# Performance work log

Hardware: AMD Instinct MI355X
Metric: run time of the kernel (lower is better)

## Reference

```python
import jax, jax.numpy as jnp
import numpy as np


def setup_inputs() -> dict:
    key = jax.random.key(0)
    k1, k2, k3 = jax.random.split(key, 3)
    B, H, W, D, K = 16, 32, 32, 128, 32
    x = jax.random.normal(k1, (B, H, W, D), dtype=jnp.float32)
    std = 1.0 / (K * D) ** 0.5
    codewords = jax.random.uniform(k2, (K, D), minval=-std, maxval=std, dtype=jnp.float32)
    scale = jax.random.uniform(k3, (K,), minval=-1.0, maxval=0.0, dtype=jnp.float32)
    return {"x": x, "codewords": codewords, "scale": scale}


def reference(x, codewords, scale):
    B, H, W, D = x.shape
    K = codewords.shape[0]
    X = x.reshape(B, H * W, D)                      # [B, N, D]
    # scaled squared distances: s_k * ||x_n - c_k||^2 via expansion (no BNKD tensor)
    x2 = jnp.sum(X * X, axis=-1, keepdims=True)     # [B, N, 1]
    c2 = jnp.sum(codewords * codewords, axis=-1)    # [K]
    xc = jnp.einsum('bnd,kd->bnk', X, codewords)    # [B, N, K]
    SL = scale[None, None, :] * (x2 - 2.0 * xc + c2[None, None, :])
    A = jax.nn.softmax(SL, axis=2)                  # assignment weights [B, N, K]
    # E_bk = sum_n A_bnk * (x_bn - c_k)
    E = jnp.einsum('bnk,bnd->bkd', A, X) - jnp.sum(A, axis=1)[:, :, None] * codewords[None]
    return E
```

## Files before the change

### kernel.cpp

```cpp
#include <hip/hip_runtime.h>


constexpr int NPB = 32;
constexpr int XS  = 132;

__global__ __launch_bounds__(256)
void enc_partial(const float* __restrict__ x, const float* __restrict__ cw,
                 const float* __restrict__ scale, float* __restrict__ ws)
{
    __shared__ float x_s[NPB * XS];
    __shared__ float A_s[NPB * 32];
    __shared__ float x2_s[NPB];
    __shared__ float asum_s[4 * 32];

    const int tid = threadIdx.x;
    const int b   = blockIdx.x >> 5;
    const int s   = blockIdx.x & 31;

    const float4* xg4 = (const float4*)(x + (size_t)(b * 1024 + s * NPB) * 128);
#pragma unroll
    for (int i = 0; i < 4; ++i) {
        int f = tid + 256 * i;
        float4 v = xg4[f];
        *(float4*)&x_s[(f >> 5) * XS + (f & 31) * 4] = v;
    }

    const int lane = tid & 63;
    const int k    = lane & 31;
    const int h    = lane >> 5;
    const int w    = tid >> 6;

    float4 cf[16];
    const float4* cw4 = (const float4*)(cw + k * 128 + h * 64);
    float c2a = 0.f, c2b = 0.f;
#pragma unroll
    for (int i = 0; i < 16; i += 2) {
        float4 c0 = cw4[i], c1 = cw4[i + 1];
        cf[i] = c0; cf[i + 1] = c1;
        c2a += c0.x * c0.x + c0.y * c0.y + c0.z * c0.z + c0.w * c0.w;
        c2b += c1.x * c1.x + c1.y * c1.y + c1.z * c1.z + c1.w * c1.w;
    }
    float c2 = c2a + c2b;
    c2 += __shfl_xor(c2, 32);
    const float sck = scale[k];

    __syncthreads();

    {
        int p = tid >> 3, q = tid & 7;
        float ss = 0.f;
#pragma unroll
        for (int i = 0; i < 4; ++i) {
            float4 v = *(const float4*)&x_s[p * XS + q * 16 + 4 * i];
            ss += v.x * v.x + v.y * v.y + v.z * v.z + v.w * v.w;
        }
        ss += __shfl_xor(ss, 1);
        ss += __shfl_xor(ss, 2);
        ss += __shfl_xor(ss, 4);
        if (q == 0) x2_s[p] = ss;
    }
    __syncthreads();

    float a_part = 0.f;
#pragma unroll
    for (int p = 0; p < 8; ++p) {
        const int n = (w << 3) + p;
        const float4* xr = (const float4*)&x_s[n * XS + h * 64];
        float xc0 = 0.f, xc1 = 0.f, xc2 = 0.f, xc3 = 0.f;
#pragma unroll
        for (int i = 0; i < 16; i += 4) {
            float4 v0 = xr[i + 0], v1 = xr[i + 1], v2 = xr[i + 2], v3 = xr[i + 3];
            xc0 += v0.x * cf[i+0].x + v0.y * cf[i+0].y + v0.z * cf[i+0].z + v0.w * cf[i+0].w;
            xc1 += v1.x * cf[i+1].x + v1.y * cf[i+1].y + v1.z * cf[i+1].z + v1.w * cf[i+1].w;
            xc2 += v2.x * cf[i+2].x + v2.y * cf[i+2].y + v2.z * cf[i+2].z + v2.w * cf[i+2].w;
            xc3 += v3.x * cf[i+3].x + v3.y * cf[i+3].y + v3.z * cf[i+3].z + v3.w * cf[i+3].w;
        }
        float xc = (xc0 + xc1) + (xc2 + xc3);
        xc += __shfl_xor(xc, 32);

        float sl = sck * (x2_s[n] - 2.f * xc + c2);
        float m = sl;
#pragma unroll
        for (int msk = 16; msk >= 1; msk >>= 1) m = fmaxf(m, __shfl_xor(m, msk));
        float e = __expf(sl - m);
        float den = e;
#pragma unroll
        for (int msk = 16; msk >= 1; msk >>= 1) den += __shfl_xor(den, msk);
        float a = e / den;
        A_s[n * 32 + k] = a;
        a_part += a;
    }
    if (h == 0) asum_s[w * 32 + k] = a_part;
    __syncthreads();

    {
        const int kg = tid >> 5;
        const int dg = tid & 31;
        float acc[4][4];
#pragma unroll
        for (int i = 0; i < 4; ++i)
#pragma unroll
            for (int j = 0; j < 4; ++j) acc[i][j] = 0.f;

#pragma unroll 8
        for (int n = 0; n < NPB; ++n) {
            float4 a4 = *(const float4*)&A_s[n * 32 + kg * 4];
            float4 x4 = *(const float4*)&x_s[n * XS + dg * 4];
            acc[0][0] += a4.x * x4.x; acc[0][1] += a4.x * x4.y;
            acc[0][2] += a4.x * x4.z; acc[0][3] += a4.x * x4.w;
            acc[1][0] += a4.y * x4.x; acc[1][1] += a4.y * x4.y;
            acc[1][2] += a4.y * x4.z; acc[1][3] += a4.y * x4.w;
            acc[2][0] += a4.z * x4.x; acc[2][1] += a4.z * x4.y;
            acc[2][2] += a4.z * x4.z; acc[2][3] += a4.z * x4.w;
            acc[3][0] += a4.w * x4.x; acc[3][1] += a4.w * x4.y;
            acc[3][2] += a4.w * x4.z; acc[3][3] += a4.w * x4.w;
        }

        float as[4];
#pragma unroll
        for (int i = 0; i < 4; ++i)
            as[i] = asum_s[kg * 4 + i] + asum_s[32 + kg * 4 + i] +
                    asum_s[64 + kg * 4 + i] + asum_s[96 + kg * 4 + i];

        float* wb = ws + (size_t)(b * 32 + s) * 4096;
#pragma unroll
        for (int i = 0; i < 4; ++i) {
            const int kk = kg * 4 + i;
            float4 c4 = *(const float4*)&cw[kk * 128 + dg * 4];
            float4 r;
            r.x = acc[i][0] - as[i] * c4.x;
            r.y = acc[i][1] - as[i] * c4.y;
            r.z = acc[i][2] - as[i] * c4.z;
            r.w = acc[i][3] - as[i] * c4.w;
            *(float4*)&wb[kk * 128 + dg * 4] = r;
        }
    }
}

__global__ __launch_bounds__(256)
void enc_reduce(const float* __restrict__ ws, float* __restrict__ out)
{
    const int gid = blockIdx.x * 256 + threadIdx.x;
    const int b   = gid >> 10;
    const int j4  = gid & 1023;
    const float4* base = (const float4*)ws + (size_t)b * 32768 + j4;
    float4 a0 = {0,0,0,0}, a1 = {0,0,0,0}, a2 = {0,0,0,0}, a3 = {0,0,0,0};
#pragma unroll
    for (int s = 0; s < 32; s += 4) {
        float4 v0 = base[(size_t)(s + 0) * 1024];
        float4 v1 = base[(size_t)(s + 1) * 1024];
        float4 v2 = base[(size_t)(s + 2) * 1024];
        float4 v3 = base[(size_t)(s + 3) * 1024];
        a0.x += v0.x; a0.y += v0.y; a0.z += v0.z; a0.w += v0.w;
        a1.x += v1.x; a1.y += v1.y; a1.z += v1.z; a1.w += v1.w;
        a2.x += v2.x; a2.y += v2.y; a2.z += v2.z; a2.w += v2.w;
        a3.x += v3.x; a3.y += v3.y; a3.z += v3.z; a3.w += v3.w;
    }
    float4 r;
    r.x = (a0.x + a1.x) + (a2.x + a3.x);
    r.y = (a0.y + a1.y) + (a2.y + a3.y);
    r.z = (a0.z + a1.z) + (a2.z + a3.z);
    r.w = (a0.w + a1.w) + (a2.w + a3.w);
    ((float4*)out)[gid] = r;
}

extern "C" void kernel_launch(void* const* d_in, const int* in_sizes, int n_in,
                              void* d_out, int out_size, void* d_ws, size_t ws_size,
                              hipStream_t stream)
{
    const float* x     = (const float*)d_in[0];
    const float* cw    = (const float*)d_in[1];
    const float* scale = (const float*)d_in[2];
    float* out = (float*)d_out;
    float* ws  = (float*)d_ws;

    enc_partial<<<512, 256, 0, stream>>>(x, cw, scale, ws);
    enc_reduce<<<64, 256, 0, stream>>>(ws, out);
}
```

Baseline: 75.94 us.

## Compute distance GEMM with register-tiled shared-memory codewords and split-D partial sums

Codewords are staged in shared memory instead of held per-thread in registers. The x·c product becomes a register-tiled 4x4 outer-product GEMM, with D split across four groups whose partial sums go to shared memory and are reduced afterwards. Softmax runs per point with 8 threads each covering 4 codewords, so fewer shuffles are needed, and the assignment sums are folded into the second GEMM loop. This trades roughly 33KB more shared memory and an extra barrier for fewer registers and better reuse in the first GEMM.

```diff
diff --git a/kernel.cpp b/kernel.cpp
--- a/kernel.cpp
+++ b/kernel.cpp
@@ -1,109 +1,131 @@
 #include <hip/hip_runtime.h>
 
 
-constexpr int NPB = 32;
-constexpr int XS  = 132;
+constexpr int XS = 132;
 
 __global__ __launch_bounds__(256)
 void enc_partial(const float* __restrict__ x, const float* __restrict__ cw,
                  const float* __restrict__ scale, float* __restrict__ ws)
 {
-    __shared__ float x_s[NPB * XS];
-    __shared__ float A_s[NPB * 32];
-    __shared__ float x2_s[NPB];
-    __shared__ float asum_s[4 * 32];
+    __shared__ float x_s[32 * XS];
+    __shared__ float c_s[32 * XS];
+    __shared__ float S_s[4 * 32 * 32];
+    __shared__ float A_s[32 * 32];
+    __shared__ float x2_s[32];
+    __shared__ float c2_s[32];
 
     const int tid = threadIdx.x;
     const int b   = blockIdx.x >> 5;
     const int s   = blockIdx.x & 31;
 
-    const float4* xg4 = (const float4*)(x + (size_t)(b * 1024 + s * NPB) * 128);
+    const float4* xg4 = (const float4*)(x + (size_t)(b * 1024 + s * 32) * 128);
+    const float4* cg4 = (const float4*)cw;
 #pragma unroll
     for (int i = 0; i < 4; ++i) {
         int f = tid + 256 * i;
-        float4 v = xg4[f];
-        *(float4*)&x_s[(f >> 5) * XS + (f & 31) * 4] = v;
+        float4 vx = xg4[f];
+        float4 vc = cg4[f];
+        *(float4*)&x_s[(f >> 5) * XS + (f & 31) * 4] = vx;
+        *(float4*)&c_s[(f >> 5) * XS + (f & 31) * 4] = vc;
     }
-
-    const int lane = tid & 63;
-    const int k    = lane & 31;
-    const int h    = lane >> 5;
-    const int w    = tid >> 6;
-
-    float4 cf[16];
-    const float4* cw4 = (const float4*)(cw + k * 128 + h * 64);
-    float c2a = 0.f, c2b = 0.f;
-#pragma unroll
-    for (int i = 0; i < 16; i += 2) {
-        float4 c0 = cw4[i], c1 = cw4[i + 1];
-        cf[i] = c0; cf[i + 1] = c1;
-        c2a += c0.x * c0.x + c0.y * c0.y + c0.z * c0.z + c0.w * c0.w;
-        c2b += c1.x * c1.x + c1.y * c1.y + c1.z * c1.z + c1.w * c1.w;
-    }
-    float c2 = c2a + c2b;
-    c2 += __shfl_xor(c2, 32);
-    const float sck = scale[k];
-
     __syncthreads();
 
     {
-        int p = tid >> 3, q = tid & 7;
-        float ss = 0.f;
+        const int p = tid >> 3, q = tid & 7;
+        float sx = 0.f, sc = 0.f;
 #pragma unroll
         for (int i = 0; i < 4; ++i) {
             float4 v = *(const float4*)&x_s[p * XS + q * 16 + 4 * i];
-            ss += v.x * v.x + v.y * v.y + v.z * v.z + v.w * v.w;
+            float4 c = *(const float4*)&c_s[p * XS + q * 16 + 4 * i];
+            sx += v.x * v.x + v.y * v.y + v.z * v.z + v.w * v.w;
+            sc += c.x * c.x + c.y * c.y + c.z * c.z + c.w * c.w;
         }
-        ss += __shfl_xor(ss, 1);
-        ss += __shfl_xor(ss, 2);
-        ss += __shfl_xor(ss, 4);
-        if (q == 0) x2_s[p] = ss;
+        sx += __shfl_xor(sx, 1); sc += __shfl_xor(sc, 1);
+        sx += __shfl_xor(sx, 2); sc += __shfl_xor(sc, 2);
+        sx += __shfl_xor(sx, 4); sc += __shfl_xor(sc, 4);
+        if (q == 0) { x2_s[p] = sx; c2_s[p] = sc; }
     }
     __syncthreads();
 
-    float a_part = 0.f;
+    {
+        const int dq = tid >> 6;
+        const int kg = (tid >> 3) & 7;
+        const int ng = tid & 7;
+        float acc[4][4];
 #pragma unroll
-    for (int p = 0; p < 8; ++p) {
-        const int n = (w << 3) + p;
-        const float4* xr = (const float4*)&x_s[n * XS + h * 64];
-        float xc0 = 0.f, xc1 = 0.f, xc2 = 0.f, xc3 = 0.f;
+        for (int r = 0; r < 4; ++r)
 #pragma unroll
-        for (int i = 0; i < 16; i += 4) {
-            float4 v0 = xr[i + 0], v1 = xr[i + 1], v2 = xr[i + 2], v3 = xr[i + 3];
-            xc0 += v0.x * cf[i+0].x + v0.y * cf[i+0].y + v0.z * cf[i+0].z + v0.w * cf[i+0].w;
-            xc1 += v1.x * cf[i+1].x + v1.y * cf[i+1].y + v1.z * cf[i+1].z + v1.w * cf[i+1].w;
-            xc2 += v2.x * cf[i+2].x + v2.y * cf[i+2].y + v2.z * cf[i+2].z + v2.w * cf[i+2].w;
-            xc3 += v3.x * cf[i+3].x + v3.y * cf[i+3].y + v3.z * cf[i+3].z + v3.w * cf[i+3].w;
+            for (int c = 0; c < 4; ++c) acc[r][c] = 0.f;
+
+#pragma unroll
+        for (int i = 0; i < 8; ++i) {
+            const int d4 = dq * 8 + i;
+            float4 xv[4], cv[4];
+#pragma unroll
+            for (int r = 0; r < 4; ++r) {
+                xv[r] = *(const float4*)&x_s[(ng * 4 + r) * XS + d4 * 4];
+                cv[r] = *(const float4*)&c_s[(kg * 4 + r) * XS + d4 * 4];
+            }
+#pragma unroll
+            for (int r = 0; r < 4; ++r)
+#pragma unroll
+                for (int c = 0; c < 4; ++c)
+                    acc[r][c] += xv[r].x * cv[c].x + xv[r].y * cv[c].y +
+                                 xv[r].z * cv[c].z + xv[r].w * cv[c].w;
         }
-        float xc = (xc0 + xc1) + (xc2 + xc3);
-        xc += __shfl_xor(xc, 32);
+#pragma unroll
+        for (int r = 0; r < 4; ++r) {
+            float4 o = {acc[r][0], acc[r][1], acc[r][2], acc[r][3]};
+            *(float4*)&S_s[(dq * 32 + ng * 4 + r) * 32 + kg * 4] = o;
+        }
+    }
+    __syncthreads();
 
-        float sl = sck * (x2_s[n] - 2.f * xc + c2);
-        float m = sl;
+    {
+        const int n = tid >> 3, j = tid & 7;
+        float4 xc = {0.f, 0.f, 0.f, 0.f};
 #pragma unroll
-        for (int msk = 16; msk >= 1; msk >>= 1) m = fmaxf(m, __shfl_xor(m, msk));
-        float e = __expf(sl - m);
-        float den = e;
-#pragma unroll
-        for (int msk = 16; msk >= 1; msk >>= 1) den += __shfl_xor(den, msk);
-        float a = e / den;
-        A_s[n * 32 + k] = a;
-        a_part += a;
+        for (int dq = 0; dq < 4; ++dq) {
+            float4 v = *(const float4*)&S_s[(dq * 32 + n) * 32 + j * 4];
+            xc.x += v.x; xc.y += v.y; xc.z += v.z; xc.w += v.w;
+        }
+        const float4 s4  = ((const float4*)scale)[j];
+        const float4 c24 = *(const float4*)&c2_s[j * 4];
+        const float x2n  = x2_s[n];
+        float4 sl;
+        sl.x = s4.x * (x2n - 2.f * xc.x + c24.x);
+        sl.y = s4.y * (x2n - 2.f * xc.y + c24.y);
+        sl.z = s4.z * (x2n - 2.f * xc.z + c24.z);
+        sl.w = s4.w * (x2n - 2.f * xc.w + c24.w);
+        float m = fmaxf(fmaxf(sl.x, sl.y), fmaxf(sl.z, sl.w));
+        m = fmaxf(m, __shfl_xor(m, 1));
+        m = fmaxf(m, __shfl_xor(m, 2));
+        m = fmaxf(m, __shfl_xor(m, 4));
+        float4 e;
+        e.x = __expf(sl.x - m); e.y = __expf(sl.y - m);
+        e.z = __expf(sl.z - m); e.w = __expf(sl.w - m);
+        float den = (e.x + e.y) + (e.z + e.w);
+        den += __shfl_xor(den, 1);
+        den += __shfl_xor(den, 2);
+        den += __shfl_xor(den, 4);
+        const float rd = 1.f / den;
+        float4 a = {e.x * rd, e.y * rd, e.z * rd, e.w * rd};
+        *(float4*)&A_s[n * 32 + j * 4] = a;
     }
-    if (h == 0) asum_s[w * 32 + k] = a_part;
     __syncthreads();
 
     {
         const int kg = tid >> 5;
         const int dg = tid & 31;
         float acc[4][4];
+        float as[4] = {0.f, 0.f, 0.f, 0.f};
 #pragma unroll
         for (int i = 0; i < 4; ++i)
 #pragma unroll
             for (int j = 0; j < 4; ++j) acc[i][j] = 0.f;
 
 #pragma unroll 8
-        for (int n = 0; n < NPB; ++n) {
+        for (int n = 0; n < 32; ++n) {
             float4 a4 = *(const float4*)&A_s[n * 32 + kg * 4];
             float4 x4 = *(const float4*)&x_s[n * XS + dg * 4];
             acc[0][0] += a4.x * x4.x; acc[0][1] += a4.x * x4.y;
@@ -114,13 +136,8 @@
             acc[2][2] += a4.z * x4.z; acc[2][3] += a4.z * x4.w;
             acc[3][0] += a4.w * x4.x; acc[3][1] += a4.w * x4.y;
             acc[3][2] += a4.w * x4.z; acc[3][3] += a4.w * x4.w;
+            as[0] += a4.x; as[1] += a4.y; as[2] += a4.z; as[3] += a4.w;
         }
-
-        float as[4];
-#pragma unroll
-        for (int i = 0; i < 4; ++i)
-            as[i] = asum_s[kg * 4 + i] + asum_s[32 + kg * 4 + i] +
-                    asum_s[64 + kg * 4 + i] + asum_s[96 + kg * 4 + i];
 
         float* wb = ws + (size_t)(b * 32 + s) * 4096;
 #pragma unroll
```

Measured after the change: 71.87 us. 1.06x faster.

## Compute x·codeword distances with bf16 MFMA instead of scalar FP32 dot products

Applied to the files above, without the earlier changes.

The block converts its x tile and the codewords to bf16 in shared memory and computes the 32x32 x·c product with a single-wave-shaped 32x32x16 bf16 MFMA chain. Each wave then takes four rows of the accumulator for the softmax. The x and codeword squared norms are computed at load time. The per-k assignment sums are now accumulated in the second matmul loop, replacing the separate shared array. This cuts FP32 FMA and register-held codeword work in the first stage, at the cost of bf16 rounding in the distance logits and redundant MFMA work across the four waves.

```diff
diff --git a/kernel.cpp b/kernel.cpp
--- a/kernel.cpp
+++ b/kernel.cpp
@@ -1,126 +1,125 @@
 #include <hip/hip_runtime.h>
 
 
-constexpr int NPB = 32;
+typedef __attribute__((ext_vector_type(8))) short bf16x8;
+typedef __attribute__((ext_vector_type(16))) float f32x16;
+
 constexpr int XS  = 132;
+constexpr int XBS = 136;
+
+__device__ __forceinline__ unsigned short f2bf(float f) {
+    unsigned u = __float_as_uint(f);
+    u += 0x7fffu + ((u >> 16) & 1u);
+    return (unsigned short)(u >> 16);
+}
 
 __global__ __launch_bounds__(256)
 void enc_partial(const float* __restrict__ x, const float* __restrict__ cw,
                  const float* __restrict__ scale, float* __restrict__ ws)
 {
-    __shared__ float x_s[NPB * XS];
-    __shared__ float A_s[NPB * 32];
-    __shared__ float x2_s[NPB];
-    __shared__ float asum_s[4 * 32];
+    __shared__ float          x_s[32 * XS];
+    __shared__ unsigned short xb_s[32 * XBS];
+    __shared__ unsigned short cb_s[32 * XBS];
+    __shared__ float          A_s[32 * 32];
+    __shared__ float          x2_s[32];
+    __shared__ float          c2_s[32];
 
     const int tid = threadIdx.x;
     const int b   = blockIdx.x >> 5;
     const int s   = blockIdx.x & 31;
 
-    const float4* xg4 = (const float4*)(x + (size_t)(b * 1024 + s * NPB) * 128);
+    const float4* xg4 = (const float4*)(x + (size_t)(b * 1024 + s * 32) * 128);
+    const float4* cg4 = (const float4*)cw;
+
 #pragma unroll
     for (int i = 0; i < 4; ++i) {
-        int f = tid + 256 * i;
-        float4 v = xg4[f];
-        *(float4*)&x_s[(f >> 5) * XS + (f & 31) * 4] = v;
-    }
-
-    const int lane = tid & 63;
-    const int k    = lane & 31;
-    const int h    = lane >> 5;
-    const int w    = tid >> 6;
-
-    float4 cf[16];
-    const float4* cw4 = (const float4*)(cw + k * 128 + h * 64);
-    float c2a = 0.f, c2b = 0.f;
+        const int f   = tid + 256 * i;
+        const int row = 8 * i + (tid >> 5);
+        const int col = tid & 31;
+        float4 vx = xg4[f];
+        float4 vc = cg4[f];
+        *(float4*)&x_s[row * XS + col * 4] = vx;
+        short4 hx = { (short)f2bf(vx.x), (short)f2bf(vx.y),
+                      (short)f2bf(vx.z), (short)f2bf(vx.w) };
+        short4 hc = { (short)f2bf(vc.x), (short)f2bf(vc.y),
+                      (short)f2bf(vc.z), (short)f2bf(vc.w) };
+        *(short4*)&xb_s[row * XBS + col * 4] = hx;
+        *(short4*)&cb_s[row * XBS + col * 4] = hc;
+        float sx = vx.x * vx.x + vx.y * vx.y + vx.z * vx.z + vx.w * vx.w;
+        float sc = vc.x * vc.x + vc.y * vc.y + vc.z * vc.z + vc.w * vc.w;
 #pragma unroll
-    for (int i = 0; i < 16; i += 2) {
-        float4 c0 = cw4[i], c1 = cw4[i + 1];
-        cf[i] = c0; cf[i + 1] = c1;
-        c2a += c0.x * c0.x + c0.y * c0.y + c0.z * c0.z + c0.w * c0.w;
-        c2b += c1.x * c1.x + c1.y * c1.y + c1.z * c1.z + c1.w * c1.w;
-    }
-    float c2 = c2a + c2b;
-    c2 += __shfl_xor(c2, 32);
-    const float sck = scale[k];
-
-    __syncthreads();
-
-    {
-        int p = tid >> 3, q = tid & 7;
-        float ss = 0.f;
-#pragma unroll
-        for (int i = 0; i < 4; ++i) {
-            float4 v = *(const float4*)&x_s[p * XS + q * 16 + 4 * i];
-            ss += v.x * v.x + v.y * v.y + v.z * v.z + v.w * v.w;
+        for (int m = 16; m >= 1; m >>= 1) {
+            sx += __shfl_xor(sx, m);
+            sc += __shfl_xor(sc, m);
         }
-        ss += __shfl_xor(ss, 1);
-        ss += __shfl_xor(ss, 2);
-        ss += __shfl_xor(ss, 4);
-        if (q == 0) x2_s[p] = ss;
+        if ((tid & 31) == 0) { x2_s[row] = sx; c2_s[row] = sc; }
     }
     __syncthreads();
 
-    float a_part = 0.f;
+    const int lc = tid & 31;
+    const int lh = (tid >> 5) & 1;
+    f32x16 acc;
 #pragma unroll
-    for (int p = 0; p < 8; ++p) {
-        const int n = (w << 3) + p;
-        const float4* xr = (const float4*)&x_s[n * XS + h * 64];
-        float xc0 = 0.f, xc1 = 0.f, xc2 = 0.f, xc3 = 0.f;
+    for (int i = 0; i < 16; ++i) acc[i] = 0.f;
 #pragma unroll
-        for (int i = 0; i < 16; i += 4) {
-            float4 v0 = xr[i + 0], v1 = xr[i + 1], v2 = xr[i + 2], v3 = xr[i + 3];
-            xc0 += v0.x * cf[i+0].x + v0.y * cf[i+0].y + v0.z * cf[i+0].z + v0.w * cf[i+0].w;
-            xc1 += v1.x * cf[i+1].x + v1.y * cf[i+1].y + v1.z * cf[i+1].z + v1.w * cf[i+1].w;
-            xc2 += v2.x * cf[i+2].x + v2.y * cf[i+2].y + v2.z * cf[i+2].z + v2.w * cf[i+2].w;
-            xc3 += v3.x * cf[i+3].x + v3.y * cf[i+3].y + v3.z * cf[i+3].z + v3.w * cf[i+3].w;
+    for (int t = 0; t < 8; ++t) {
+        bf16x8 af = *(const bf16x8*)&xb_s[lc * XBS + t * 16 + lh * 8];
+        bf16x8 bfr = *(const bf16x8*)&cb_s[lc * XBS + t * 16 + lh * 8];
+        acc = __builtin_amdgcn_mfma_f32_32x32x16_bf16(af, bfr, acc, 0, 0, 0);
+    }
+
+    {
+        const int w = tid >> 6;
+        const float sck = scale[lc];
+        const float c2k = c2_s[lc];
+        const float4 x2v = *(const float4*)&x2_s[8 * w + 4 * lh];
+        float sl[4] = {
+            sck * (x2v.x - 2.f * acc[4 * w + 0] + c2k),
+            sck * (x2v.y - 2.f * acc[4 * w + 1] + c2k),
+            sck * (x2v.z - 2.f * acc[4 * w + 2] + c2k),
+            sck * (x2v.w - 2.f * acc[4 * w + 3] + c2k) };
+        float a[4];
+#pragma unroll
+        for (int q = 0; q < 4; ++q) {
+            float m = sl[q];
+#pragma unroll
+            for (int msk = 16; msk >= 1; msk >>= 1) m = fmaxf(m, __shfl_xor(m, msk));
+            float e = __expf(sl[q] - m);
+            float den = e;
+#pragma unroll
+            for (int msk = 16; msk >= 1; msk >>= 1) den += __shfl_xor(den, msk);
+            a[q] = e / den;
         }
-        float xc = (xc0 + xc1) + (xc2 + xc3);
-        xc += __shfl_xor(xc, 32);
-
-        float sl = sck * (x2_s[n] - 2.f * xc + c2);
-        float m = sl;
 #pragma unroll
-        for (int msk = 16; msk >= 1; msk >>= 1) m = fmaxf(m, __shfl_xor(m, msk));
-        float e = __expf(sl - m);
-        float den = e;
-#pragma unroll
-        for (int msk = 16; msk >= 1; msk >>= 1) den += __shfl_xor(den, msk);
-        float a = e / den;
-        A_s[n * 32 + k] = a;
-        a_part += a;
+        for (int q = 0; q < 4; ++q)
+            A_s[(q + 8 * w + 4 * lh) * 32 + lc] = a[q];
     }
-    if (h == 0) asum_s[w * 32 + k] = a_part;
     __syncthreads();
 
     {
         const int kg = tid >> 5;
         const int dg = tid & 31;
-        float acc[4][4];
+        float pacc[4][4];
+        float as[4] = {0.f, 0.f, 0.f, 0.f};
 #pragma unroll
         for (int i = 0; i < 4; ++i)
 #pragma unroll
-            for (int j = 0; j < 4; ++j) acc[i][j] = 0.f;
+            for (int j = 0; j < 4; ++j) pacc[i][j] = 0.f;
 
 #pragma unroll 8
-        for (int n = 0; n < NPB; ++n) {
+        for (int n = 0; n < 32; ++n) {
             float4 a4 = *(const float4*)&A_s[n * 32 + kg * 4];
             float4 x4 = *(const float4*)&x_s[n * XS + dg * 4];
-            acc[0][0] += a4.x * x4.x; acc[0][1] += a4.x * x4.y;
-            acc[0][2] += a4.x * x4.z; acc[0][3] += a4.x * x4.w;
-            acc[1][0] += a4.y * x4.x; acc[1][1] += a4.y * x4.y;
-            acc[1][2] += a4.y * x4.z; acc[1][3] += a4.y * x4.w;
-            acc[2][0] += a4.z * x4.x; acc[2][1] += a4.z * x4.y;
-            acc[2][2] += a4.z * x4.z; acc[2][3] += a4.z * x4.w;
-            acc[3][0] += a4.w * x4.x; acc[3][1] += a4.w * x4.y;
-            acc[3][2] += a4.w * x4.z; acc[3][3] += a4.w * x4.w;
+            pacc[0][0] += a4.x * x4.x; pacc[0][1] += a4.x * x4.y;
+            pacc[0][2] += a4.x * x4.z; pacc[0][3] += a4.x * x4.w;
+            pacc[1][0] += a4.y * x4.x; pacc[1][1] += a4.y * x4.y;
+            pacc[1][2] += a4.y * x4.z; pacc[1][3] += a4.y * x4.w;
+            pacc[2][0] += a4.z * x4.x; pacc[2][1] += a4.z * x4.y;
+            pacc[2][2] += a4.z * x4.z; pacc[2][3] += a4.z * x4.w;
+            pacc[3][0] += a4.w * x4.x; pacc[3][1] += a4.w * x4.y;
+            pacc[3][2] += a4.w * x4.z; pacc[3][3] += a4.w * x4.w;
+            as[0] += a4.x; as[1] += a4.y; as[2] += a4.z; as[3] += a4.w;
         }
-
-        float as[4];
-#pragma unroll
-        for (int i = 0; i < 4; ++i)
-            as[i] = asum_s[kg * 4 + i] + asum_s[32 + kg * 4 + i] +
-                    asum_s[64 + kg * 4 + i] + asum_s[96 + kg * 4 + i];
 
         float* wb = ws + (size_t)(b * 32 + s) * 4096;
 #pragma unroll
@@ -128,10 +127,10 @@
             const int kk = kg * 4 + i;
             float4 c4 = *(const float4*)&cw[kk * 128 + dg * 4];
             float4 r;
-            r.x = acc[i][0] - as[i] * c4.x;
-            r.y = acc[i][1] - as[i] * c4.y;
-            r.z = acc[i][2] - as[i] * c4.z;
-            r.w = acc[i][3] - as[i] * c4.w;
+            r.x = pacc[i][0] - as[i] * c4.x;
+            r.y = pacc[i][1] - as[i] * c4.y;
+            r.z = pacc[i][2] - as[i] * c4.z;
+            r.w = pacc[i][3] - as[i] * c4.w;
             *(float4*)&wb[kk * 128 + dg * 4] = r;
         }
     }
```

Result: faster. 71.11 us (-6.4%).
